# Kernel optimization log

Measured on AMD Instinct MI355X. Metric: run time of the kernel, lower is better.

## Reference

```python
import jax, jax.numpy as jnp
import numpy as np


def _conv(x, w, b=None, stride=1, pad=0):
    y = jax.lax.conv_general_dilated(
        x, w, (stride, stride), [(pad, pad), (pad, pad)],
        dimension_numbers=('NCHW', 'OIHW', 'NCHW'))
    if b is not None:
        y = y + b[None, :, None, None]
    return y


def _cam(x, gamma):
    # channel self-attention: energy[b,c,d] = <x[b,c,:], x[b,d,:]>
    B, C, H, W = x.shape
    xf = x.reshape(B, C, H * W)
    energy = jnp.einsum('bcn,bdn->bcd', xf, xf)                 # [B,C,C]
    energy_new = jnp.max(energy, -1, keepdims=True) - energy
    att = jax.nn.softmax(energy_new, axis=-1)
    out = jnp.einsum('bcd,bdn->bcn', att, xf).reshape(B, C, H, W)
    return gamma * out + x


def setup_inputs() -> dict:
    key = jax.random.key(0)
    ks = jax.random.split(key, 16)
    B = 16
    c2 = jax.random.normal(ks[0], (B, 512, 64, 64), jnp.float32)
    c3 = jax.random.normal(ks[1], (B, 1024, 32, 32), jnp.float32)
    c4 = jax.random.normal(ks[2], (B, 2048, 16, 16), jnp.float32)
    s = lambda fan: 1.0 / np.sqrt(fan)
    # CAM_4: 1x1 conv 2048->512 (bias)
    w4 = jax.random.normal(ks[3], (512, 2048, 1, 1), jnp.float32) * s(2048)
    b4 = jax.random.normal(ks[4], (512,), jnp.float32) * 0.01
    # CAM_3: 3x3 stride-2 conv 1024->512 (no bias)
    w3 = jax.random.normal(ks[5], (512, 1024, 3, 3), jnp.float32) * s(1024 * 9)
    # CAM_2: two 3x3 stride-2 convs 512->512 (first no bias, second bias)
    w2a = jax.random.normal(ks[6], (512, 512, 3, 3), jnp.float32) * s(512 * 9)
    w2b = jax.random.normal(ks[7], (512, 512, 3, 3), jnp.float32) * s(512 * 9)
    b2b = jax.random.normal(ks[8], (512,), jnp.float32) * 0.01
    # gammas (nn.Parameter(zeros(1)) in original; small nonzero to exercise the branch)
    g2 = jax.random.normal(ks[9], (1,), jnp.float32) * 0.1
    g3 = jax.random.normal(ks[10], (1,), jnp.float32) * 0.1
    g4 = jax.random.normal(ks[11], (1,), jnp.float32) * 0.1
    # final FC: (2048 + 512*3) -> 2
    fc_w = jax.random.normal(ks[12], (2, 3584), jnp.float32) * s(3584)
    fc_b = jax.random.normal(ks[13], (2,), jnp.float32) * 0.01
    return {'c2': c2, 'c3': c3, 'c4': c4, 'w4': w4, 'b4': b4, 'w3': w3,
            'w2a': w2a, 'w2b': w2b, 'b2b': b2b, 'g2': g2, 'g3': g3, 'g4': g4,
            'fc_w': fc_w, 'fc_b': fc_b}


def reference(c2, c3, c4, w4, b4, w3, w2a, w2b, b2b, g2, g3, g4, fc_w, fc_b):
    # CAM_4: flag=True, MS=True
    out4 = _cam(c4, g4)
    pam4 = _conv(out4, w4, b4)                  # [B,512,16,16]
    down4 = _conv(c4, w4, b4)                   # x1 = conv(c4)
    cam4 = pam4 + down4
    # CAM_3: flag=False -> down3 = down4
    out3 = _cam(c3, g3)
    pam3 = _conv(out3, w3, stride=2, pad=1)     # [B,512,16,16]
    cam3 = pam3 + down4
    # CAM_2: flag=False -> x1 stays down4
    out2 = _cam(c2, g2)
    pam2 = _conv(_conv(out2, w2a, stride=2, pad=1), w2b, b2b, stride=2, pad=1)
    cam2 = pam2 + down4
    feat = jnp.concatenate([cam2, cam3, cam4, c4], axis=1)   # [B,3584,16,16]
    pooled = feat.mean(axis=(2, 3))                          # adaptive avg pool 1x1
    return pooled @ fc_w.T + fc_b                            # [B,2]
```

## Files before the change

kernel.cpp:

```cpp
#include <hip/hip_runtime.h>

typedef _Float16 h8 __attribute__((ext_vector_type(8)));
typedef float f4 __attribute__((ext_vector_type(4)));

#define DEVINL __device__ __forceinline__


DEVINL void gload_lds(const _Float16* g, _Float16* l)
{
    __builtin_amdgcn_global_load_lds(
        (const __attribute__((address_space(1))) void*)g,
        (__attribute__((address_space(3))) void*)l, 16, 0, 0);
}


DEVINL void vtb_write(_Float16* vtb, int CB, int p, int d, float v)
{
    size_t off = (((size_t)(p >> 4) * CB) + (d >> 5)) * 512
               + (size_t)(((d >> 3) & 3) * 16 + (p & 15)) * 8 + (d & 7);
    vtb[off] = (_Float16)v;
}

extern "C" __global__ __launch_bounds__(256)
void func_c4_kernel(const float* __restrict__ x, _Float16* __restrict__ vtb,
                    float* __restrict__ V4d)
{
    int wave = threadIdx.x >> 6, lane = threadIdx.x & 63;
    int idx = blockIdx.x * 4 + wave;
    int b = idx >> 11, i = idx & 2047;
    size_t base = (size_t)(b * 2048 + i) * 256;
    float acc = 0.f;
#pragma unroll
    for (int it = 0; it < 4; ++it) acc += x[base + it * 64 + lane];
#pragma unroll
    for (int m = 1; m < 64; m <<= 1) acc += __shfl_xor(acc, m);
    float mean = acc * (1.f / 256.f);
    _Float16* vb = vtb + (size_t)b * 16 * 2048;
    if (lane < 16) vtb_write(vb, 64, lane, i, (lane == 0) ? mean : 0.f);
    if (lane == 0) V4d[b * 2048 + i] = mean;
}

extern "C" __global__ __launch_bounds__(256)
void func_c3_kernel(const float* __restrict__ x, _Float16* __restrict__ vtb)
{
    __shared__ float scr[4][12];
    int wave = threadIdx.x >> 6, lane = threadIdx.x & 63;
    int idx = blockIdx.x * 4 + wave;
    int b = idx >> 10, i = idx & 1023;
    size_t base = (size_t)(b * 1024 + i) * 1024;
    float acc = 0.f;
    for (int it = 0; it < 15; ++it) acc += x[base + it * 64 + lane];
    float vl = x[base + 15 * 64 + lane];
    acc += vl;
    float tr = (lane >= 32) ? vl : 0.f;
    float tcpre = acc;
    float xpre = tr;
#pragma unroll
    for (int m = 2; m < 32; m <<= 1) {
        acc += __shfl_xor(acc, m);
        tr += __shfl_xor(tr, m);
    }
    if ((lane & 31) < 2) {
        int rp = lane >> 5, cp = lane & 1;
        scr[wave][rp * 2 + cp] = acc;
        if (rp == 1) scr[wave][4 + cp] = tr;
    }
    if ((lane & 31) == 31) {
        int rp = lane >> 5;
        scr[wave][6 + rp] = tcpre;
        if (rp == 1) scr[wave][8] = xpre;
    }
    __syncthreads();
    if (lane < 16) {
        float out = 0.f;
        if (lane < 9) {
            int kh = lane / 3, kw = lane - kh * 3;
            int rp = (kh == 1) ? 0 : 1, cp = (kw == 1) ? 0 : 1;
            bool er = (kh == 0), ec = (kw == 0);
            const float* s = scr[wave];
            out = s[rp * 2 + cp];
            if (er) out -= s[4 + cp];
            if (ec) out -= s[6 + rp];
            if (er && ec) out += s[8];
        }
        vtb_write(vtb + (size_t)b * 16 * 1024, 32, lane, i, out);
    }
}

DEVINL float camU(const float* s, int p)
{
    int rc = p / 9, cc = p - rc * 9;
    int kh = rc / 3, kh2 = rc - kh * 3;
    int kw = cc / 3, kw2 = cc - kw * 3;
    int rm = (kh == 1) ? ((kh2 + 3) & 3) : (kh2 + 1);
    int cm = (kw == 1) ? ((kw2 + 3) & 3) : (kw2 + 1);
    bool er = (rc < 4), ec = (cc < 4);
    float u = s[rm * 4 + cm];
    if (er) u -= s[16 + (rm - 1) * 4 + cm];
    if (ec) u -= s[28 + rm * 3 + (cm - 1)];
    if (er && ec) u += s[40 + (rm - 1) * 3 + (cm - 1)];
    return u;
}

extern "C" __global__ __launch_bounds__(256)
void func_c2_kernel(const float* __restrict__ x, _Float16* __restrict__ vtb)
{
    __shared__ float scr[4][52];
    int wave = threadIdx.x >> 6, lane = threadIdx.x & 63;
    int idx = blockIdx.x * 4 + wave;
    int b = idx >> 9, i = idx & 511;
    size_t base = (size_t)(b * 512 + i) * 4096;
    float acc[4] = {0.f, 0.f, 0.f, 0.f};
    float tr[3];
    for (int it = 0; it < 60; it += 4) {
#pragma unroll
        for (int rr = 0; rr < 4; ++rr)
            acc[rr] += x[base + (size_t)(it + rr) * 64 + lane];
    }
    acc[0] += x[base + 60 * 64 + lane];
#pragma unroll
    for (int rr = 1; rr < 4; ++rr) {
        float v = x[base + (size_t)(60 + rr) * 64 + lane];
        acc[rr] += v;
        tr[rr - 1] = v;
    }
    float tcx[4], xr[3];
#pragma unroll
    for (int g = 0; g < 4; ++g) tcx[g] = acc[g];
#pragma unroll
    for (int g = 0; g < 3; ++g) xr[g] = tr[g];
#pragma unroll
    for (int m = 4; m < 64; m <<= 1) {
#pragma unroll
        for (int g = 0; g < 4; ++g) acc[g] += __shfl_xor(acc[g], m);
#pragma unroll
        for (int g = 0; g < 3; ++g) tr[g] += __shfl_xor(tr[g], m);
    }
    if (lane < 4) {
#pragma unroll
        for (int rm = 0; rm < 4; ++rm) scr[wave][rm * 4 + lane] = acc[rm];
#pragma unroll
        for (int rx = 0; rx < 3; ++rx) scr[wave][16 + rx * 4 + lane] = tr[rx];
    }
    if (lane >= 61) {
        int cx = lane - 61;
#pragma unroll
        for (int rm = 0; rm < 4; ++rm) scr[wave][28 + rm * 3 + cx] = tcx[rm];
#pragma unroll
        for (int rx = 0; rx < 3; ++rx) scr[wave][40 + rx * 3 + cx] = xr[rx];
    }
    __syncthreads();
    const float* s = scr[wave];
    _Float16* vb = vtb + (size_t)b * 96 * 512;
    vtb_write(vb, 16, lane, i, camU(s, lane));
    if (lane < 32) {
        int p = 64 + lane;
        vtb_write(vb, 16, p, i, (p < 81) ? camU(s, p) : 0.f);
    }
}

DEVINL void repack_tile(const float* __restrict__ src, _Float16* __restrict__ dst,
                        int K, int grp, int chunk, _Float16 (*T)[264])
{
    int tid = threadIdx.x;
    {
        int row = tid >> 4, t16 = tid & 15;
        const float* s = src + ((size_t)grp * 16 + row) * K + chunk * 256 + t16 * 16;
        float4 a = *(const float4*)(s + 0);
        float4 b = *(const float4*)(s + 4);
        float4 c = *(const float4*)(s + 8);
        float4 d = *(const float4*)(s + 12);
        h8 lo = {(_Float16)a.x, (_Float16)a.y, (_Float16)a.z, (_Float16)a.w,
                 (_Float16)b.x, (_Float16)b.y, (_Float16)b.z, (_Float16)b.w};
        h8 hi = {(_Float16)c.x, (_Float16)c.y, (_Float16)c.z, (_Float16)c.w,
                 (_Float16)d.x, (_Float16)d.y, (_Float16)d.z, (_Float16)d.w};
        *(h8*)&T[row][t16 * 16] = lo;
        *(h8*)&T[row][t16 * 16 + 8] = hi;
    }
    __syncthreads();
    int fl = tid >> 5, idx2 = tid & 31;
    size_t base = (size_t)grp * 16 * K + (size_t)(chunk * 8 + fl) * 512;
#pragma unroll
    for (int rep = 0; rep < 2; ++rep) {
        int idx = idx2 + rep * 32;
        int l16 = idx & 15, quad = idx >> 4;
        h8 v = *(h8*)&T[l16][fl * 32 + quad * 8];
        *(h8*)&dst[base + (size_t)idx * 8] = v;
    }
}

extern "C" __global__ __launch_bounds__(256)
void repack_kernel(const float* __restrict__ c2, const float* __restrict__ c3,
                   const float* __restrict__ c4, _Float16* __restrict__ xb2,
                   _Float16* __restrict__ xb3, _Float16* __restrict__ xb4)
{
    __shared__ _Float16 T[16][264];
    int bid = blockIdx.x;
    const float* src; _Float16* dst; int K, grp, chunk;
    if (bid < 8192) { src = c2; dst = xb2; K = 4096; grp = bid >> 4; chunk = bid & 15; }
    else if (bid < 12288) { int id = bid - 8192; src = c3; dst = xb3; K = 1024; grp = id >> 2; chunk = id & 3; }
    else { src = c4; dst = xb4; K = 256; grp = bid - 12288; chunk = 0; }
    repack_tile(src, dst, K, grp, chunk, T);
}

extern "C" __global__ __launch_bounds__(256)
void repack_w_kernel(const float* __restrict__ w4, const float* __restrict__ w3,
                     const float* __restrict__ w2a, const float* __restrict__ w2b,
                     _Float16* __restrict__ w4f, _Float16* __restrict__ w3f,
                     _Float16* __restrict__ w2af, _Float16* __restrict__ w2bf)
{
    __shared__ _Float16 T[16][264];
    int bid = blockIdx.x;
    const float* src; _Float16* dst; int K, grp, chunk;
    if (bid < 256) { src = w4; dst = w4f; K = 2048; grp = bid >> 3; chunk = bid & 7; }
    else if (bid < 1408) { int t = bid - 256; src = w3; dst = w3f; K = 9216; grp = t / 36; chunk = t - 36 * (t / 36); }
    else if (bid < 1984) { int t = bid - 1408; src = w2a; dst = w2af; K = 4608; grp = t / 18; chunk = t - 18 * (t / 18); }
    else { int t = bid - 1984; src = w2b; dst = w2bf; K = 4608; grp = t / 18; chunk = t - 18 * (t / 18); }
    repack_tile(src, dst, K, grp, chunk, T);
}

template <int N, int C, int DT, int MODE, int RT>
DEVINL void flashT(const _Float16* __restrict__ xfb, const _Float16* __restrict__ vtb,
                   float* __restrict__ Fout, float* __restrict__ FoutD,
                   _Float16* __restrict__ Wg, float* __restrict__ Sml,
                   const float* __restrict__ gptr, int r0, int c0,
                   _Float16* SB, _Float16* SWw)
{
    static_assert(RT == 2, "vmcnt(2) invariant assumes 2 anxt loads per wave");
    constexpr int KB = N >> 5;
    const int lane = threadIdx.x & 63;
    const int wave = threadIdx.x >> 6;
    const int l16 = lane & 15, quad = lane >> 4;
    const f4 fz = {0.f, 0.f, 0.f, 0.f};
    const size_t loff = (size_t)lane * 8;

    const _Float16* Abase = xfb + (size_t)((r0 >> 4) + wave * RT) * KB * 512 + loff;

    f4 accp[RT];
    float m_run[RT][4], l_run[RT][4];
#pragma unroll
    for (int rt = 0; rt < RT; ++rt) {
        accp[rt] = fz;
#pragma unroll
        for (int g = 0; g < 4; ++g) { m_run[rt][g] = -3.0e38f; l_run[rt][g] = 0.f; }
    }

    h8 acur[RT], anxt[RT];
    {
        int fr = wave * 2;
#pragma unroll
        for (int u = 0; u < 2; ++u)
            gload_lds(xfb + (size_t)(((c0 >> 4) + fr + u) * KB) * 512 + loff,
                      SB + ((size_t)(fr + u) << 9));
    }
    __builtin_amdgcn_sched_barrier(0);
#pragma unroll
    for (int rt = 0; rt < RT; ++rt)
        acur[rt] = *(const h8*)(Abase + (size_t)rt * KB * 512);

    for (int dt = 0; dt < DT; ++dt) {
        const int d0 = c0 + dt * 128;
        f4 e[RT][8];
#pragma unroll
        for (int rt = 0; rt < RT; ++rt)
#pragma unroll
            for (int ct = 0; ct < 8; ++ct) e[rt][ct] = fz;

#pragma unroll 2
        for (int kc = 0; kc < KB; ++kc) {
            const int buf = kc & 1;
            asm volatile("s_waitcnt vmcnt(2)" ::: "memory");
            __builtin_amdgcn_s_barrier();
            __builtin_amdgcn_sched_barrier(0);
            if (!((dt == DT - 1) && (kc == KB - 1))) {
                int nkb = (kc == KB - 1) ? 0 : kc + 1;
                int nd0 = (kc == KB - 1) ? d0 + 128 : d0;
                int fr = wave * 2;
#pragma unroll
                for (int u = 0; u < 2; ++u)
                    gload_lds(xfb + (size_t)(((nd0 >> 4) + fr + u) * KB + nkb) * 512 + loff,
                              SB + ((size_t)((buf ^ 1) * 8 + fr + u) << 9));
                __builtin_amdgcn_sched_barrier(0);
#pragma unroll
                for (int rt = 0; rt < RT; ++rt)
                    anxt[rt] = *(const h8*)(Abase + ((size_t)rt * KB + nkb) * 512);
            }
#pragma unroll
            for (int ct = 0; ct < 8; ++ct) {
                h8 bf = *(const h8*)&SB[((size_t)(buf * 8 + ct) << 9) + loff];
#pragma unroll
                for (int rt = 0; rt < RT; ++rt)
                    e[rt][ct] = __builtin_amdgcn_mfma_f32_16x16x32_f16(acur[rt], bf, e[rt][ct], 0, 0, 0);
            }
#pragma unroll
            for (int rt = 0; rt < RT; ++rt) acur[rt] = anxt[rt];
        }

#pragma unroll
        for (int rt = 0; rt < RT; ++rt) {
            float mx[4];
#pragma unroll
            for (int g = 0; g < 4; ++g) {
                float v = -e[rt][0][g];
#pragma unroll
                for (int ct = 1; ct < 8; ++ct) v = fmaxf(v, -e[rt][ct][g]);
                mx[g] = v;
            }
#pragma unroll
            for (int m = 1; m < 16; m <<= 1)
#pragma unroll
                for (int g = 0; g < 4; ++g) mx[g] = fmaxf(mx[g], __shfl_xor(mx[g], m));
            float mref[4], al[4];
            if (MODE != 3) {
#pragma unroll
                for (int g = 0; g < 4; ++g) {
                    float nm = fmaxf(m_run[rt][g], mx[g]);
                    al[g] = __expf(m_run[rt][g] - nm);
                    m_run[rt][g] = nm;
                    mref[g] = nm;
                    accp[rt][g] *= al[g];
                }
            } else {
#pragma unroll
                for (int g = 0; g < 4; ++g) mref[g] = mx[g];
            }
            float rs[4] = {0.f, 0.f, 0.f, 0.f};
#pragma unroll
            for (int ct = 0; ct < 8; ++ct) {
#pragma unroll
                for (int g = 0; g < 4; ++g) {
                    float w = __expf(-e[rt][ct][g] - mref[g]);
                    rs[g] += w;
                    int lane2 = ((ct * 2 + (l16 >> 3)) & 3) * 16 + quad * 4 + g;
                    SWw[((ct >> 1) << 9) + lane2 * 8 + (l16 & 7)] = (_Float16)w;
                }
            }
#pragma unroll
            for (int kc2 = 0; kc2 < 4; ++kc2) {
                h8 wa = *(const h8*)&SWw[((size_t)kc2 << 9) + loff];
                if (MODE == 3) {
                    int tile = (c0 >> 7) + dt;
                    int rfrag = (r0 >> 4) + wave * RT + rt;
                    *(h8*)&Wg[((size_t)((tile * 32 + rfrag) * 4 + kc2) << 9) + loff] = wa;
                } else {
                    h8 vb = *(const h8*)(vtb + (((size_t)(d0 >> 5) + kc2) << 9) + loff);
                    accp[rt] = __builtin_amdgcn_mfma_f32_16x16x32_f16(wa, vb, accp[rt], 0, 0, 0);
                }
            }
#pragma unroll
            for (int m = 1; m < 16; m <<= 1)
#pragma unroll
                for (int g = 0; g < 4; ++g) rs[g] += __shfl_xor(rs[g], m);
            if (MODE == 3) {
                if (l16 == 0) {
                    int tile = (c0 >> 7) + dt;
#pragma unroll
                    for (int g = 0; g < 4; ++g) {
                        int row = r0 + wave * (16 * RT) + rt * 16 + quad * 4 + g;
                        Sml[((size_t)tile * 512 + row) * 2 + 0] = mref[g];
                        Sml[((size_t)tile * 512 + row) * 2 + 1] = rs[g];
                    }
                }
            } else {
#pragma unroll
                for (int g = 0; g < 4; ++g)
                    l_run[rt][g] = l_run[rt][g] * al[g] + rs[g];
            }
        }
    }
    if (MODE == 1) {
        float gam = gptr[0];
#pragma unroll
        for (int rt = 0; rt < RT; ++rt)
#pragma unroll
            for (int g = 0; g < 4; ++g) {
                int row = r0 + wave * (16 * RT) + rt * 16 + quad * 4 + g;
                float ident = (float)vtb[(size_t)(row >> 5) * 512
                               + (size_t)(((row >> 3) & 3) * 16 + l16) * 8 + (row & 7)];
                Fout[(size_t)row * 16 + l16] = gam * (accp[rt][g] / l_run[rt][g]) + ident;
            }
    } else if (MODE == 2) {
        float gam = gptr[0];
        if (l16 == 0) {
#pragma unroll
            for (int rt = 0; rt < RT; ++rt)
#pragma unroll
                for (int g = 0; g < 4; ++g) {
                    int row = r0 + wave * (16 * RT) + rt * 16 + quad * 4 + g;
                    float ident = (float)vtb[(size_t)(row >> 5) * 512
                                   + (size_t)(((row >> 3) & 3) * 16) * 8 + (row & 7)];
                    FoutD[row] = gam * (accp[rt][g] / l_run[rt][g]) + ident;
                }
        }
    }
}

extern "C" __global__ __launch_bounds__(256, 3)
void flash_kernel(const _Float16* __restrict__ xb2, const _Float16* __restrict__ xb3,
                  const _Float16* __restrict__ xb4,
                  const _Float16* __restrict__ V3, const _Float16* __restrict__ V4,
                  _Float16* __restrict__ Wg, float* __restrict__ Sml,
                  float* __restrict__ F3, float* __restrict__ F4d,
                  const float* __restrict__ g3, const float* __restrict__ g4)
{
    __shared__ _Float16 SB[16 * 512];
    __shared__ _Float16 SW[4 * 4 * 512];
    _Float16* SWw = &SW[(threadIdx.x >> 6) * 4 * 512];
    int bid = blockIdx.x;
    if (bid < 128) {
        int t = bid, x = t & 7, u = t >> 3;
        int b = x + 8 * (u & 1), rb = u >> 1;
        flashT<1024, 1024, 8, 1, 2>(xb3 + (size_t)b * 1024 * 1024, V3 + (size_t)b * 16 * 1024,
                                    F3 + (size_t)b * 1024 * 16, nullptr, nullptr, nullptr, g3,
                                    rb * 128, 0, SB, SWw);
    } else if (bid < 384) {
        int t = bid - 128, x = t & 7, u = t >> 3;
        int b = x + 8 * (u & 1), unit = u >> 1;
        int rb = unit & 3, ds = unit >> 2;
        flashT<4096, 512, 1, 3, 2>(xb2 + (size_t)b * 512 * 4096, nullptr, nullptr, nullptr,
                                   Wg + (size_t)b * 262144, Sml + (size_t)b * 4096, nullptr,
                                   rb * 128, ds * 128, SB, SWw);
    } else {
        int t = bid - 384, x = t & 7, u = t >> 3;
        int b = x + 8 * (u & 1), rb = u >> 1;
        flashT<256, 2048, 16, 2, 2>(xb4 + (size_t)b * 2048 * 256, V4 + (size_t)b * 16 * 2048,
                                    nullptr, F4d + (size_t)b * 2048, nullptr, nullptr, g4,
                                    rb * 128, 0, SB, SWw);
    }
}

extern "C" __global__ __launch_bounds__(256)
void proj_c2_kernel(const _Float16* __restrict__ Wg, const float* __restrict__ Sml,
                    const _Float16* __restrict__ V2, const float* __restrict__ g2,
                    float* __restrict__ F2)
{
    int b = blockIdx.x >> 2, rb = blockIdx.x & 3;
    int lane = threadIdx.x & 63, wave = threadIdx.x >> 6;
    int l16 = lane & 15, quad = lane >> 4;
    size_t loff = (size_t)lane * 8;
    const _Float16* Wb = Wg + (size_t)b * 262144;
    const float* Sb = Sml + (size_t)b * 4096;
    const _Float16* Vb = V2 + (size_t)b * 96 * 512;
    const f4 fz = {0.f, 0.f, 0.f, 0.f};
    f4 accP[2][6];
    float M[2][4], L[2][4];
#pragma unroll
    for (int rt = 0; rt < 2; ++rt) {
#pragma unroll
        for (int pt = 0; pt < 6; ++pt) accP[rt][pt] = fz;
#pragma unroll
        for (int g = 0; g < 4; ++g) { M[rt][g] = -3.0e38f; L[rt][g] = 0.f; }
    }
    for (int t = 0; t < 4; ++t) {
        f4 tmp[2][6];
#pragma unroll
        for (int rt = 0; rt < 2; ++rt)
#pragma unroll
            for (int pt = 0; pt < 6; ++pt) tmp[rt][pt] = fz;
#pragma unroll
        for (int kb = 0; kb < 4; ++kb) {
            h8 wa[2];
#pragma unroll
            for (int rt = 0; rt < 2; ++rt) {
                int rfrag = rb * 8 + wave * 2 + rt;
                wa[rt] = *(const h8*)&Wb[((size_t)((t * 32 + rfrag) * 4 + kb) << 9) + loff];
            }
#pragma unroll
            for (int pt = 0; pt < 6; ++pt) {
                h8 vb = *(const h8*)&Vb[((size_t)(pt * 16 + t * 4 + kb) << 9) + loff];
#pragma unroll
                for (int rt = 0; rt < 2; ++rt)
                    tmp[rt][pt] = __builtin_amdgcn_mfma_f32_16x16x32_f16(wa[rt], vb, tmp[rt][pt], 0, 0, 0);
            }
        }
#pragma unroll
        for (int rt = 0; rt < 2; ++rt)
#pragma unroll
            for (int g = 0; g < 4; ++g) {
                int row = (rb * 8 + wave * 2 + rt) * 16 + quad * 4 + g;
                float mt = Sb[((size_t)t * 512 + row) * 2 + 0];
                float lt = Sb[((size_t)t * 512 + row) * 2 + 1];
                float nm = fmaxf(M[rt][g], mt);
                float ao = __expf(M[rt][g] - nm);
                float at = __expf(mt - nm);
#pragma unroll
                for (int pt = 0; pt < 6; ++pt)
                    accP[rt][pt][g] = accP[rt][pt][g] * ao + at * tmp[rt][pt][g];
                L[rt][g] = L[rt][g] * ao + at * lt;
                M[rt][g] = nm;
            }
    }
    float gam = g2[0];
#pragma unroll
    for (int rt = 0; rt < 2; ++rt)
#pragma unroll
        for (int pt = 0; pt < 6; ++pt)
#pragma unroll
            for (int g = 0; g < 4; ++g) {
                int row = (rb * 8 + wave * 2 + rt) * 16 + quad * 4 + g;
                int p = pt * 16 + l16;
                float ident = (float)Vb[((size_t)pt * 16 + (row >> 5)) * 512
                               + (size_t)(((row >> 3) & 3) * 16 + (p & 15)) * 8 + (row & 7)];
                F2[((size_t)b * 512 + row) * 96 + p] = gam * (accP[rt][pt][g] / L[rt][g]) + ident;
            }
}

extern "C" __global__ __launch_bounds__(256)
void gather1_kernel(const float* __restrict__ F2, const float* __restrict__ F3,
                    const float* __restrict__ V4d, const float* __restrict__ F4d,
                    _Float16* __restrict__ G, _Float16* __restrict__ XB3,
                    _Float16* __restrict__ XB4)
{
    int gid = blockIdx.x * 256 + threadIdx.x;
    int lane = gid & 63, fragid = gid >> 6;
    int kq = lane >> 4, n16 = lane & 15;
    _Float16 v[8];
    if (fragid < 1296) {
        int nb = fragid / 144, kb = fragid - nb * 144;
        int n = nb * 16 + n16;
        int b = n / 9, kcol = n - b * 9;
        int kh = kcol / 3, kw = kcol - kh * 3;
#pragma unroll
        for (int j = 0; j < 8; ++j) {
            int K = kb * 32 + kq * 8 + j;
            int i = K / 9, k2 = K - i * 9;
            int kh2 = k2 / 3, kw2 = k2 - kh2 * 3;
            int p = (kh * 3 + kh2) * 9 + kw * 3 + kw2;
            v[j] = (_Float16)F2[((size_t)b * 512 + i) * 96 + p];
        }
        *(h8*)&G[((size_t)fragid << 9) + lane * 8] = *(h8*)v;
    } else if (fragid < 1584) {
        int kb = fragid - 1296;
#pragma unroll
        for (int j = 0; j < 8; ++j) {
            int K = kb * 32 + kq * 8 + j;
            int i = K / 9, k9 = K - i * 9;
            v[j] = (_Float16)F3[((size_t)n16 * 1024 + i) * 16 + k9];
        }
        *(h8*)&XB3[((size_t)kb << 9) + lane * 8] = *(h8*)v;
    } else {
        int f = fragid - 1584;
        int nb = f >> 6, kb = f & 63;
        const float* src = nb ? F4d : V4d;
#pragma unroll
        for (int j = 0; j < 8; ++j) {
            int i = kb * 32 + kq * 8 + j;
            v[j] = (_Float16)src[(size_t)n16 * 2048 + i];
        }
        *(h8*)&XB4[((size_t)f << 9) + lane * 8] = *(h8*)v;
    }
}

extern "C" __global__ __launch_bounds__(256)
void gather2_kernel(const float* __restrict__ Pv, _Float16* __restrict__ XB2)
{
    int gid = blockIdx.x * 256 + threadIdx.x;
    int lane = gid & 63, kb = gid >> 6;
    int kq = lane >> 4, b = lane & 15;
    _Float16 v[8];
#pragma unroll
    for (int j = 0; j < 8; ++j) {
        int K = kb * 32 + kq * 8 + j;
        int jj = K / 9, k = K - jj * 9;
        float s = 0.f;
#pragma unroll
        for (int ss = 0; ss < 9; ++ss)
            s += Pv[((size_t)ss * 8192 + (size_t)b * 512 + jj) * 9 + k];
        v[j] = (_Float16)s;
    }
    *(h8*)&XB2[((size_t)kb << 9) + lane * 8] = *(h8*)v;
}

extern "C" __global__ __launch_bounds__(256)
void ep_gemm1_kernel(const _Float16* __restrict__ w2af, const _Float16* __restrict__ G,
                     const _Float16* __restrict__ w3f, const _Float16* __restrict__ XB3,
                     const _Float16* __restrict__ w4f, const _Float16* __restrict__ XB4,
                     float* __restrict__ Pv, float* __restrict__ Pr3,
                     float* __restrict__ Pr4)
{
    int lane = threadIdx.x & 63, wave = threadIdx.x >> 6;
    int l16 = lane & 15, quad = lane >> 4;
    size_t loff = (size_t)lane * 8;
    const f4 fz = {0.f, 0.f, 0.f, 0.f};
    int bid = blockIdx.x;
    if (bid < 72) {
        int unit = bid * 4 + wave;
        int mt = unit & 31, s = unit >> 5;
        f4 acc[9];
#pragma unroll
        for (int nb = 0; nb < 9; ++nb) acc[nb] = fz;
#pragma unroll 2
        for (int kf = s * 16; kf < s * 16 + 16; ++kf) {
            h8 a = *(const h8*)&w2af[(((size_t)(mt * 144 + kf)) << 9) + loff];
#pragma unroll
            for (int nb = 0; nb < 9; ++nb) {
                h8 bfr = *(const h8*)&G[(((size_t)(nb * 144 + kf)) << 9) + loff];
                acc[nb] = __builtin_amdgcn_mfma_f32_16x16x32_f16(a, bfr, acc[nb], 0, 0, 0);
            }
        }
#pragma unroll
        for (int nb = 0; nb < 9; ++nb)
#pragma unroll
            for (int g = 0; g < 4; ++g) {
                int j = mt * 16 + quad * 4 + g;
                int n = nb * 16 + l16;
                int b = n / 9, k = n - b * 9;
                Pv[((size_t)s * 8192 + (size_t)b * 512 + j) * 9 + k] = acc[nb][g];
            }
    } else if (bid < 216) {
        int unit = (bid - 72) * 4 + wave;
        int mt = unit & 31, s = unit >> 5;
        f4 acc = fz;
#pragma unroll 4
        for (int kf = s * 16; kf < s * 16 + 16; ++kf) {
            h8 a = *(const h8*)&w3f[(((size_t)(mt * 288 + kf)) << 9) + loff];
            h8 bfr = *(const h8*)&XB3[((size_t)kf << 9) + loff];
            acc = __builtin_amdgcn_mfma_f32_16x16x32_f16(a, bfr, acc, 0, 0, 0);
        }
#pragma unroll
        for (int g = 0; g < 4; ++g)
            Pr3[(size_t)(s * 512 + mt * 16 + quad * 4 + g) * 16 + l16] = acc[g];
    } else {
        int unit = (bid - 216) * 4 + wave;
        int mt = unit & 31, s = unit >> 5;
        f4 acc[2] = {fz, fz};
#pragma unroll 2
        for (int kf = s * 8; kf < s * 8 + 8; ++kf) {
            h8 a = *(const h8*)&w4f[(((size_t)(mt * 64 + kf)) << 9) + loff];
#pragma unroll
            for (int nb = 0; nb < 2; ++nb) {
                h8 bfr = *(const h8*)&XB4[(((size_t)(nb * 64 + kf)) << 9) + loff];
                acc[nb] = __builtin_amdgcn_mfma_f32_16x16x32_f16(a, bfr, acc[nb], 0, 0, 0);
            }
        }
#pragma unroll
        for (int nb = 0; nb < 2; ++nb)
#pragma unroll
            for (int g = 0; g < 4; ++g)
                Pr4[((size_t)s * 1024 + (size_t)nb * 512 + mt * 16 + quad * 4 + g) * 16 + l16] = acc[nb][g];
    }
}

extern "C" __global__ __launch_bounds__(256)
void ep_gemm2_kernel(const _Float16* __restrict__ w2bf, const _Float16* __restrict__ XB2,
                     float* __restrict__ Pr2)
{
    int lane = threadIdx.x & 63, wave = threadIdx.x >> 6;
    int l16 = lane & 15, quad = lane >> 4;
    size_t loff = (size_t)lane * 8;
    int unit = blockIdx.x * 4 + wave;
    int mt = unit & 31, s = unit >> 5;
    f4 acc = {0.f, 0.f, 0.f, 0.f};
#pragma unroll 4
    for (int kf = s * 16; kf < s * 16 + 16; ++kf) {
        h8 a = *(const h8*)&w2bf[(((size_t)(mt * 144 + kf)) << 9) + loff];
        h8 bfr = *(const h8*)&XB2[((size_t)kf << 9) + loff];
        acc = __builtin_amdgcn_mfma_f32_16x16x32_f16(a, bfr, acc, 0, 0, 0);
    }
#pragma unroll
    for (int g = 0; g < 4; ++g)
        Pr2[(size_t)(s * 512 + mt * 16 + quad * 4 + g) * 16 + l16] = acc[g];
}

extern "C" __global__ __launch_bounds__(256)
void final_kernel(const float* __restrict__ Pr2, const float* __restrict__ Pr3,
                  const float* __restrict__ Pr4, const float* __restrict__ V4d,
                  const float* __restrict__ b4, const float* __restrict__ b2b,
                  const float* __restrict__ fcw, const float* __restrict__ fcb,
                  float* __restrict__ out)
{
    __shared__ float pf[3584];
    __shared__ float r0s[256], r1s[256];
    int b = blockIdx.x, tid = threadIdx.x;
    for (int o = tid; o < 512; o += 256) {
        float pd = 0.f, pa = 0.f;
#pragma unroll
        for (int s = 0; s < 8; ++s) {
            pd += Pr4[(size_t)(s * 1024 + o) * 16 + b];
            pa += Pr4[(size_t)(s * 1024 + 512 + o) * 16 + b];
        }
        float r3 = 0.f;
#pragma unroll
        for (int s = 0; s < 18; ++s) r3 += Pr3[(size_t)(s * 512 + o) * 16 + b];
        float r2 = 0.f;
#pragma unroll
        for (int s = 0; s < 9; ++s) r2 += Pr2[(size_t)(s * 512 + o) * 16 + b];
        float pd4 = pd + b4[o];
        pf[1024 + o] = pa + b4[o] + pd4;
        pf[512 + o] = r3 * (1.f / 256.f) + pd4;
        pf[o] = r2 * (1.f / 256.f) + b2b[o] + pd4;
    }
    for (int i = tid; i < 2048; i += 256) pf[1536 + i] = V4d[(size_t)b * 2048 + i];
    __syncthreads();
    float p0 = 0.f, p1 = 0.f;
    for (int k = tid; k < 3584; k += 256) {
        float f = pf[k];
        p0 += fcw[k] * f;
        p1 += fcw[3584 + k] * f;
    }
    r0s[tid] = p0;
    r1s[tid] = p1;
    __syncthreads();
    for (int s = 128; s > 0; s >>= 1) {
        if (tid < s) { r0s[tid] += r0s[tid + s]; r1s[tid] += r1s[tid + s]; }
        __syncthreads();
    }
    if (tid == 0) {
        out[b * 2 + 0] = r0s[0] + fcb[0];
        out[b * 2 + 1] = r1s[0] + fcb[1];
    }
}


extern "C" void kernel_launch(void* const* d_in, const int* in_sizes, int n_in,
                              void* d_out, int out_size, void* d_ws, size_t ws_size,
                              hipStream_t stream)
{
    const float* c2 = (const float*)d_in[0];
    const float* c3 = (const float*)d_in[1];
    const float* c4 = (const float*)d_in[2];
    const float* w4 = (const float*)d_in[3];
    const float* b4 = (const float*)d_in[4];
    const float* w3 = (const float*)d_in[5];
    const float* w2a = (const float*)d_in[6];
    const float* w2b = (const float*)d_in[7];
    const float* b2b = (const float*)d_in[8];
    const float* g2 = (const float*)d_in[9];
    const float* g3 = (const float*)d_in[10];
    const float* g4 = (const float*)d_in[11];
    const float* fcw = (const float*)d_in[12];
    const float* fcb = (const float*)d_in[13];
    float* out = (float*)d_out;

    char* ws = (char*)d_ws;
    size_t off = 0;
    auto carve = [&](size_t bytes) -> char* {
        char* p = ws + off;
        off += (bytes + 255) & ~(size_t)255;
        return p;
    };
    _Float16* xb2 = (_Float16*)carve(67108864);
    _Float16* xb3 = (_Float16*)carve(33554432);
    _Float16* xb4 = (_Float16*)carve(16777216);
    _Float16* V2 = (_Float16*)carve(1572864);
    _Float16* V3 = (_Float16*)carve(524288);
    _Float16* V4 = (_Float16*)carve(1048576);
    float* V4d = (float*)carve(131072);
    _Float16* Wg = (_Float16*)carve(8388608);
    float* Sml = (float*)carve(262144);
    float* F3 = (float*)carve(1048576);
    float* F4d = (float*)carve(131072);
    if (ws_size < off) return;

    char* al = (char*)xb2;
    auto sub = [&](size_t bytes) -> char* {
        char* p = al;
        al += (bytes + 255) & ~(size_t)255;
        return p;
    };
    float* F2 = (float*)sub(3145728);
    _Float16* w4f = (_Float16*)sub(2097152);
    _Float16* w3f = (_Float16*)sub(9437184);
    _Float16* w2af = (_Float16*)sub(4718592);
    _Float16* w2bf = (_Float16*)sub(4718592);
    _Float16* G = (_Float16*)sub(1327104);
    _Float16* XB3 = (_Float16*)sub(294912);
    _Float16* XB4 = (_Float16*)sub(131072);
    float* Pv = (float*)sub(2654208);
    _Float16* XB2 = (_Float16*)sub(147456);
    float* Pr2 = (float*)sub(294912);
    float* Pr3 = (float*)sub(589824);
    float* Pr4 = (float*)sub(524288);

    repack_kernel<<<14336, 256, 0, stream>>>(c2, c3, c4, xb2, xb3, xb4);
    func_c2_kernel<<<2048, 256, 0, stream>>>(c2, V2);
    func_c3_kernel<<<4096, 256, 0, stream>>>(c3, V3);
    func_c4_kernel<<<8192, 256, 0, stream>>>(c4, V4, V4d);
    flash_kernel<<<640, 256, 0, stream>>>(xb2, xb3, xb4, V3, V4, Wg, Sml,
                                          F3, F4d, g3, g4);
    repack_w_kernel<<<2560, 256, 0, stream>>>(w4, w3, w2a, w2b, w4f, w3f, w2af, w2bf);
    proj_c2_kernel<<<64, 256, 0, stream>>>(Wg, Sml, V2, g2, F2);
    gather1_kernel<<<428, 256, 0, stream>>>(F2, F3, V4d, F4d, G, XB3, XB4);
    ep_gemm1_kernel<<<280, 256, 0, stream>>>(w2af, G, w3f, XB3, w4f, XB4,
                                             Pv, Pr3, Pr4);
    gather2_kernel<<<36, 256, 0, stream>>>(Pv, XB2);
    ep_gemm2_kernel<<<72, 256, 0, stream>>>(w2bf, XB2, Pr2);
    final_kernel<<<16, 256, 0, stream>>>(Pr2, Pr3, Pr4, V4d, b4, b2b,
                                         fcw, fcb, out);
}
```

Before: 673.4 us.

## Flatten flash loop and deepen LDS prefetch to quad-buffered distance two

Merges the nested dt/kc loops of the flash-attention style kernel into one flat loop over all K chunks. The LDS staging of B fragments now uses four buffers and issues global-to-LDS loads two iterations ahead instead of one. The V fragments for the second MFMA are loaded into registers at the start of each d-tile instead of inside the softmax epilogue. This is meant to hide global load latency better and remove the pipeline drain at d-tile boundaries. In exchange LDS use doubles, which may lower occupancy under launch_bounds(256,3), and the vmcnt(2) accounting now has more loads in flight.

```diff
diff --git a/kernel.cpp b/kernel.cpp
--- a/kernel.cpp
+++ b/kernel.cpp
@@ -226,13 +226,15 @@
                    const float* __restrict__ gptr, int r0, int c0,
                    _Float16* SB, _Float16* SWw)
 {
-    static_assert(RT == 2, "vmcnt(2) invariant assumes 2 anxt loads per wave");
+    static_assert(RT == 2, "vmcnt invariant assumes 2 A loads per wave");
     constexpr int KB = N >> 5;
+    constexpr int T = DT * KB;
     const int lane = threadIdx.x & 63;
     const int wave = threadIdx.x >> 6;
     const int l16 = lane & 15, quad = lane >> 4;
     const f4 fz = {0.f, 0.f, 0.f, 0.f};
     const size_t loff = (size_t)lane * 8;
+    const int fr = wave * 2;
 
     const _Float16* Abase = xfb + (size_t)((r0 >> 4) + wave * RT) * KB * 512 + loff;
 
@@ -245,46 +247,61 @@
         for (int g = 0; g < 4; ++g) { m_run[rt][g] = -3.0e38f; l_run[rt][g] = 0.f; }
     }
 
-    h8 acur[RT], anxt[RT];
-    {
-        int fr = wave * 2;
+    h8 acur[RT], anxt[RT], vbs[4];
+    f4 e[RT][8];
+
+#pragma unroll
+    for (int rt = 0; rt < RT; ++rt)
+        acur[rt] = *(const h8*)(Abase + (size_t)(rt * KB) * 512);
+    __builtin_amdgcn_sched_barrier(0);
+#pragma unroll
+    for (int u = 0; u < 2; ++u)
+        gload_lds(xfb + (size_t)(((c0 >> 4) + fr + u) * KB + 0) * 512 + loff,
+                  SB + ((size_t)(0 * 8 + fr + u) << 9));
+    if (T > 1) {
 #pragma unroll
         for (int u = 0; u < 2; ++u)
-            gload_lds(xfb + (size_t)(((c0 >> 4) + fr + u) * KB) * 512 + loff,
-                      SB + ((size_t)(fr + u) << 9));
+            gload_lds(xfb + (size_t)(((c0 >> 4) + fr + u) * KB + 1) * 512 + loff,
+                      SB + ((size_t)(1 * 8 + fr + u) << 9));
     }
     __builtin_amdgcn_sched_barrier(0);
-#pragma unroll
-    for (int rt = 0; rt < RT; ++rt)
-        acur[rt] = *(const h8*)(Abase + (size_t)rt * KB * 512);
-
-    for (int dt = 0; dt < DT; ++dt) {
-        const int d0 = c0 + dt * 128;
-        f4 e[RT][8];
-#pragma unroll
-        for (int rt = 0; rt < RT; ++rt)
-#pragma unroll
-            for (int ct = 0; ct < 8; ++ct) e[rt][ct] = fz;
-
-#pragma unroll 2
-        for (int kc = 0; kc < KB; ++kc) {
-            const int buf = kc & 1;
-            asm volatile("s_waitcnt vmcnt(2)" ::: "memory");
-            __builtin_amdgcn_s_barrier();
-            __builtin_amdgcn_sched_barrier(0);
-            if (!((dt == DT - 1) && (kc == KB - 1))) {
-                int nkb = (kc == KB - 1) ? 0 : kc + 1;
-                int nd0 = (kc == KB - 1) ? d0 + 128 : d0;
-                int fr = wave * 2;
-#pragma unroll
-                for (int u = 0; u < 2; ++u)
-                    gload_lds(xfb + (size_t)(((nd0 >> 4) + fr + u) * KB + nkb) * 512 + loff,
-                              SB + ((size_t)((buf ^ 1) * 8 + fr + u) << 9));
-                __builtin_amdgcn_sched_barrier(0);
-#pragma unroll
-                for (int rt = 0; rt < RT; ++rt)
-                    anxt[rt] = *(const h8*)(Abase + ((size_t)rt * KB + nkb) * 512);
-            }
+
+#pragma unroll 4
+    for (int t = 0; t < T; ++t) {
+        if ((t & (KB - 1)) == 0) {
+#pragma unroll
+            for (int rt = 0; rt < RT; ++rt)
+#pragma unroll
+                for (int ct = 0; ct < 8; ++ct) e[rt][ct] = fz;
+        }
+        asm volatile("s_waitcnt vmcnt(2)" ::: "memory");
+        __builtin_amdgcn_s_barrier();
+        __builtin_amdgcn_sched_barrier(0);
+        if (t + 1 < T) {
+            int nkb = (t + 1) & (KB - 1);
+#pragma unroll
+            for (int rt = 0; rt < RT; ++rt)
+                anxt[rt] = *(const h8*)(Abase + ((size_t)rt * KB + nkb) * 512);
+        }
+        if (MODE != 3 && (t & (KB - 1)) == 0) {
+            int d0 = c0 + (t / KB) * 128;
+#pragma unroll
+            for (int k2 = 0; k2 < 4; ++k2)
+                vbs[k2] = *(const h8*)(vtb + (((size_t)(d0 >> 5) + k2) << 9) + loff);
+        }
+        __builtin_amdgcn_sched_barrier(0);
+        if (t + 2 < T) {
+            int tt = t + 2;
+            int nkb = tt & (KB - 1);
+            int nd0 = c0 + (tt / KB) * 128;
+#pragma unroll
+            for (int u = 0; u < 2; ++u)
+                gload_lds(xfb + (size_t)(((nd0 >> 4) + fr + u) * KB + nkb) * 512 + loff,
+                          SB + ((size_t)((tt & 3) * 8 + fr + u) << 9));
+        }
+        __builtin_amdgcn_sched_barrier(0);
+        {
+            const int buf = t & 3;
 #pragma unroll
             for (int ct = 0; ct < 8; ++ct) {
                 h8 bf = *(const h8*)&SB[((size_t)(buf * 8 + ct) << 9) + loff];
@@ -292,79 +309,81 @@
                 for (int rt = 0; rt < RT; ++rt)
                     e[rt][ct] = __builtin_amdgcn_mfma_f32_16x16x32_f16(acur[rt], bf, e[rt][ct], 0, 0, 0);
             }
-#pragma unroll
-            for (int rt = 0; rt < RT; ++rt) acur[rt] = anxt[rt];
-        }
-
-#pragma unroll
-        for (int rt = 0; rt < RT; ++rt) {
-            float mx[4];
-#pragma unroll
-            for (int g = 0; g < 4; ++g) {
-                float v = -e[rt][0][g];
-#pragma unroll
-                for (int ct = 1; ct < 8; ++ct) v = fmaxf(v, -e[rt][ct][g]);
-                mx[g] = v;
-            }
-#pragma unroll
-            for (int m = 1; m < 16; m <<= 1)
-#pragma unroll
-                for (int g = 0; g < 4; ++g) mx[g] = fmaxf(mx[g], __shfl_xor(mx[g], m));
-            float mref[4], al[4];
-            if (MODE != 3) {
+        }
+#pragma unroll
+        for (int rt = 0; rt < RT; ++rt) acur[rt] = anxt[rt];
+
+        if ((t & (KB - 1)) == (KB - 1)) {
+            const int dt = t / KB;
+#pragma unroll
+            for (int rt = 0; rt < RT; ++rt) {
+                float mx[4];
 #pragma unroll
                 for (int g = 0; g < 4; ++g) {
-                    float nm = fmaxf(m_run[rt][g], mx[g]);
-                    al[g] = __expf(m_run[rt][g] - nm);
-                    m_run[rt][g] = nm;
-                    mref[g] = nm;
-                    accp[rt][g] *= al[g];
+                    float v = -e[rt][0][g];
+#pragma unroll
+                    for (int ct = 1; ct < 8; ++ct) v = fmaxf(v, -e[rt][ct][g]);
+                    mx[g] = v;
                 }
-            } else {
-#pragma unroll
-                for (int g = 0; g < 4; ++g) mref[g] = mx[g];
-            }
-            float rs[4] = {0.f, 0.f, 0.f, 0.f};
-#pragma unroll
-            for (int ct = 0; ct < 8; ++ct) {
-#pragma unroll
-                for (int g = 0; g < 4; ++g) {
-                    float w = __expf(-e[rt][ct][g] - mref[g]);
-                    rs[g] += w;
-                    int lane2 = ((ct * 2 + (l16 >> 3)) & 3) * 16 + quad * 4 + g;
-                    SWw[((ct >> 1) << 9) + lane2 * 8 + (l16 & 7)] = (_Float16)w;
+#pragma unroll
+                for (int m = 1; m < 16; m <<= 1)
+#pragma unroll
+                    for (int g = 0; g < 4; ++g) mx[g] = fmaxf(mx[g], __shfl_xor(mx[g], m));
+                float mref[4], al[4];
+                if (MODE != 3) {
+#pragma unroll
+                    for (int g = 0; g < 4; ++g) {
+                        float nm = fmaxf(m_run[rt][g], mx[g]);
+                        al[g] = __expf(m_run[rt][g] - nm);
+                        m_run[rt][g] = nm;
+                        mref[g] = nm;
+                        accp[rt][g] *= al[g];
+                    }
+                } else {
+#pragma unroll
+                    for (int g = 0; g < 4; ++g) mref[g] = mx[g];
                 }
-            }
-#pragma unroll
-            for (int kc2 = 0; kc2 < 4; ++kc2) {
-                h8 wa = *(const h8*)&SWw[((size_t)kc2 << 9) + loff];
-                if (MODE == 3) {
-                    int tile = (c0 >> 7) + dt;
-                    int rfrag = (r0 >> 4) + wave * RT + rt;
-                    *(h8*)&Wg[((size_t)((tile * 32 + rfrag) * 4 + kc2) << 9) + loff] = wa;
-                } else {
-                    h8 vb = *(const h8*)(vtb + (((size_t)(d0 >> 5) + kc2) << 9) + loff);
-                    accp[rt] = __builtin_amdgcn_mfma_f32_16x16x32_f16(wa, vb, accp[rt], 0, 0, 0);
-                }
-            }
-#pragma unroll
-            for (int m = 1; m < 16; m <<= 1)
-#pragma unroll
-                for (int g = 0; g < 4; ++g) rs[g] += __shfl_xor(rs[g], m);
-            if (MODE == 3) {
-                if (l16 == 0) {
-                    int tile = (c0 >> 7) + dt;
+                float rs[4] = {0.f, 0.f, 0.f, 0.f};
+#pragma unroll
+                for (int ct = 0; ct < 8; ++ct) {
 #pragma unroll
                     for (int g = 0; g < 4; ++g) {
-                        int row = r0 + wave * (16 * RT) + rt * 16 + quad * 4 + g;
-                        Sml[((size_t)tile * 512 + row) * 2 + 0] = mref[g];
-                        Sml[((size_t)tile * 512 + row) * 2 + 1] = rs[g];
+                        float w = __expf(-e[rt][ct][g] - mref[g]);
+                        rs[g] += w;
+                        int lane2 = ((ct * 2 + (l16 >> 3)) & 3) * 16 + quad * 4 + g;
+                        SWw[((ct >> 1) << 9) + lane2 * 8 + (l16 & 7)] = (_Float16)w;
                     }
                 }
-            } else {
-#pragma unroll
-                for (int g = 0; g < 4; ++g)
-                    l_run[rt][g] = l_run[rt][g] * al[g] + rs[g];
+#pragma unroll
+                for (int kc2 = 0; kc2 < 4; ++kc2) {
+                    h8 wa = *(const h8*)&SWw[((size_t)kc2 << 9) + loff];
+                    if (MODE == 3) {
+                        int tile = (c0 >> 7) + dt;
+                        int rfrag = (r0 >> 4) + wave * RT + rt;
+                        *(h8*)&Wg[((size_t)((tile * 32 + rfrag) * 4 + kc2) << 9) + loff] = wa;
+                    } else {
+                        accp[rt] = __builtin_amdgcn_mfma_f32_16x16x32_f16(wa, vbs[kc2], accp[rt], 0, 0, 0);
+                    }
+                }
+#pragma unroll
+                for (int m = 1; m < 16; m <<= 1)
+#pragma unroll
+                    for (int g = 0; g < 4; ++g) rs[g] += __shfl_xor(rs[g], m);
+                if (MODE == 3) {
+                    if (l16 == 0) {
+                        int tile = (c0 >> 7) + dt;
+#pragma unroll
+                        for (int g = 0; g < 4; ++g) {
+                            int row = r0 + wave * (16 * RT) + rt * 16 + quad * 4 + g;
+                            Sml[((size_t)tile * 512 + row) * 2 + 0] = mref[g];
+                            Sml[((size_t)tile * 512 + row) * 2 + 1] = rs[g];
+                        }
+                    }
+                } else {
+#pragma unroll
+                    for (int g = 0; g < 4; ++g)
+                        l_run[rt][g] = l_run[rt][g] * al[g] + rs[g];
+                }
             }
         }
     }
@@ -403,7 +422,7 @@
                   float* __restrict__ F3, float* __restrict__ F4d,
                   const float* __restrict__ g3, const float* __restrict__ g4)
 {
-    __shared__ _Float16 SB[16 * 512];
+    __shared__ _Float16 SB[32 * 512];
     __shared__ _Float16 SW[4 * 4 * 512];
     _Float16* SWw = &SW[(threadIdx.x >> 6) * 4 * 512];
     int bid = blockIdx.x;
```

Result: faster. 659.1 us (median of 2 runs) (-2.1%).
